# Performance work log

Hardware: AMD Instinct MI355X
Metric: run time of the kernel (lower is better)

The kernel has to match this reference:

```python
import jax, jax.numpy as jnp
import numpy as np

WINDOW_SIZE = (4, 7, 7)  # (t, h, w); N = 4*7*7 = 196


def _relative_position_index(ws):
    t, h, w = ws
    coords = np.stack(np.meshgrid(np.arange(t), np.arange(h), np.arange(w), indexing='ij'))  # (3,t,h,w)
    cf = coords.reshape(3, -1)                      # (3, N)
    rc = (cf[:, :, None] - cf[:, None, :]).transpose(1, 2, 0).astype(np.int64)  # (N, N, 3)
    rc[..., 0] += t - 1
    rc[..., 1] += h - 1
    rc[..., 2] += w - 1
    rc[..., 0] *= (2 * h - 1) * (2 * w - 1)
    rc[..., 1] *= 2 * w - 1
    return rc.sum(-1)                               # (N, N) indices into bias table


def setup_inputs() -> dict:
    key = jax.random.key(0)
    ks = jax.random.split(key, 7)
    B, B_dim, N, C, H = 4, 64, 196, 512, 16
    hd = C // H
    B_ = B * B_dim
    n_bias = (2 * 4 - 1) * (2 * 7 - 1) * (2 * 7 - 1)  # 1183
    return {
        'x': jax.random.normal(ks[0], (B_, N, C), jnp.float32),
        'q_global': jax.random.normal(ks[1], (B, 1, H, N, hd), jnp.float32),
        'kv_w': jax.random.normal(ks[2], (2 * C, C), jnp.float32) * (C ** -0.5),
        'kv_b': jnp.zeros((2 * C,), jnp.float32),
        'proj_w': jax.random.normal(ks[3], (C, C), jnp.float32) * (C ** -0.5),
        'proj_b': jnp.zeros((C,), jnp.float32),
        'bias_table': jax.random.normal(ks[4], (n_bias, H), jnp.float32) * 0.02,
    }


def reference(x, q_global, kv_w, kv_b, proj_w, proj_b, bias_table):
    B_, N, C = x.shape
    B, _, H, _, hd = q_global.shape
    B_dim = B_ // B
    scale = hd ** -0.5

    # kv projection: (B_, N, 2C) -> k, v each (B_, H, N, hd)
    kv = (x @ kv_w.T + kv_b).reshape(B_, N, 2, H, hd).transpose(2, 0, 3, 1, 4)
    keys, values = kv[0], kv[1]

    # global queries repeated across windows: (B,1,H,N,hd) -> (B_, H, N, hd)
    q = jnp.broadcast_to(q_global, (B, B_dim, H, N, hd)).reshape(B_, H, N, hd)
    q = q * scale

    attn = jnp.einsum('bhnd,bhmd->bhnm', q, keys)  # (B_, H, N, N)

    # gathered relative position bias (static index table)
    rpi = jnp.asarray(_relative_position_index(WINDOW_SIZE))  # (N, N)
    bias = bias_table[rpi.reshape(-1)].reshape(N, N, H).transpose(2, 0, 1)  # (H, N, N)
    attn = jax.nn.softmax(attn + bias[None], axis=-1)

    out = jnp.einsum('bhnm,bhmd->bhnd', attn, values)  # (B_, H, N, hd)
    out = out.transpose(0, 2, 1, 3).reshape(B_, N, C)
    return out @ proj_w.T + proj_b
```

## Files before the change

kernel.cpp:

```cpp
#include <hip/hip_runtime.h>
#include <stdint.h>

typedef __attribute__((ext_vector_type(8))) short short8;
typedef __attribute__((ext_vector_type(4))) float f32x4;
typedef __attribute__((ext_vector_type(4))) unsigned short u16x4;

typedef unsigned short ushort_t;

__device__ __forceinline__ unsigned short f2bf(float f) {
    union { float f; uint32_t u; } c; c.f = f;
    uint32_t u = c.u;
    return (unsigned short)((u + 0x7FFFu + ((u >> 16) & 1u)) >> 16);
}

__device__ __forceinline__ f32x4 mfma16(short8 a, short8 b, f32x4 c) {
    return __builtin_amdgcn_mfma_f32_16x16x32_bf16(a, b, c, 0, 0, 0);
}


__global__ __launch_bounds__(256) void cvt_x_k(const float4* __restrict__ in,
                                               u16x4* __restrict__ out, int n4) {
    int i = blockIdx.x * 256 + threadIdx.x;
    if (i < n4) {
        float4 v = in[i];
        u16x4 o;
        o[0] = f2bf(v.x); o[1] = f2bf(v.y); o[2] = f2bf(v.z); o[3] = f2bf(v.w);
        out[i] = o;
    }
}

__global__ __launch_bounds__(256) void cvt_small_k(const float4* __restrict__ kvw,
                                                   const float4* __restrict__ pw,
                                                   const float4* __restrict__ qg,
                                                   u16x4* __restrict__ kvwb,
                                                   u16x4* __restrict__ pwb,
                                                   u16x4* __restrict__ qb) {
    const float qs = 0.17677669529663687f;
    int i = blockIdx.x * 256 + threadIdx.x;
    if (i < 131072) {
        float4 v = kvw[i];
        u16x4 o; o[0]=f2bf(v.x); o[1]=f2bf(v.y); o[2]=f2bf(v.z); o[3]=f2bf(v.w);
        kvwb[i] = o;
    } else if (i < 196608) {
        int j = i - 131072;
        float4 v = pw[j];
        u16x4 o; o[0]=f2bf(v.x); o[1]=f2bf(v.y); o[2]=f2bf(v.z); o[3]=f2bf(v.w);
        pwb[j] = o;
    } else {
        int j = i - 196608;
        float4 v = qg[j];
        u16x4 o; o[0]=f2bf(v.x*qs); o[1]=f2bf(v.y*qs); o[2]=f2bf(v.z*qs); o[3]=f2bf(v.w*qs);
        qb[j] = o;
    }
}

__global__ __launch_bounds__(256) void bias_k(const float* __restrict__ bt,
                                              float* __restrict__ out) {
    int idx = blockIdx.x * 256 + threadIdx.x;
    int h = idx / 43264;
    int rem = idx - h * 43264;
    int i = rem / 208;
    int j = rem - i * 208;
    float v = -1e30f;
    if (i < 196 && j < 196) {
        int t1 = i / 49, r1 = i - t1 * 49, h1 = r1 / 7, w1 = r1 - h1 * 7;
        int t2 = j / 49, r2 = j - t2 * 49, h2 = r2 / 7, w2 = r2 - h2 * 7;
        int bi = (t1 - t2 + 3) * 169 + (h1 - h2 + 6) * 13 + (w1 - w2 + 6);
        v = bt[bi * 16 + h];
    }
    out[idx] = v;
}

__global__ __launch_bounds__(256) void gemm_kv(const ushort_t* __restrict__ A,
                                               const ushort_t* __restrict__ Bw,
                                               const float* __restrict__ kvb,
                                               ushort_t* __restrict__ Ko,
                                               ushort_t* __restrict__ Vo) {
    __shared__ ushort_t As[128 * 72];
    __shared__ ushort_t Bs[128 * 72];
    const int tid = threadIdx.x;
    const int lane = tid & 63, wave = tid >> 6;
    const int lrow = lane & 15, quad = lane >> 4;
    const int wr = wave >> 1, wc = wave & 1;
    const long arow0 = (long)blockIdx.x * 128;
    const int brow0 = blockIdx.y * 128;

    f32x4 acc[4][4];
#pragma unroll
    for (int i = 0; i < 4; ++i)
#pragma unroll
        for (int j = 0; j < 4; ++j) acc[i][j] = (f32x4){0.f, 0.f, 0.f, 0.f};

    for (int k0 = 0; k0 < 512; k0 += 64) {
        short8 ar[4], br[4];
#pragma unroll
        for (int it = 0; it < 4; ++it) {
            int c = it * 256 + tid;
            int row = c >> 3, cc = c & 7;
            ar[it] = *(const short8*)&A[(arow0 + row) * 512 + k0 + cc * 8];
            br[it] = *(const short8*)&Bw[(long)(brow0 + row) * 512 + k0 + cc * 8];
        }
        __syncthreads();
#pragma unroll
        for (int it = 0; it < 4; ++it) {
            int c = it * 256 + tid;
            int row = c >> 3, cc = c & 7;
            *(short8*)&As[row * 72 + cc * 8] = ar[it];
            *(short8*)&Bs[row * 72 + cc * 8] = br[it];
        }
        __syncthreads();
#pragma unroll
        for (int kk = 0; kk < 64; kk += 32) {
            short8 af[4], bf[4];
#pragma unroll
            for (int i = 0; i < 4; ++i)
                af[i] = *(const short8*)&As[(wr * 64 + i * 16 + lrow) * 72 + kk + quad * 8];
#pragma unroll
            for (int j = 0; j < 4; ++j)
                bf[j] = *(const short8*)&Bs[(wc * 64 + j * 16 + lrow) * 72 + kk + quad * 8];
#pragma unroll
            for (int i = 0; i < 4; ++i)
#pragma unroll
                for (int j = 0; j < 4; ++j)
                    acc[i][j] = mfma16(af[i], bf[j], acc[i][j]);
        }
    }
#pragma unroll
    for (int i = 0; i < 4; ++i) {
        int mb = (int)arow0 + wr * 64 + i * 16 + quad * 4;
#pragma unroll
        for (int r = 0; r < 4; ++r) {
            int m = mb + r;
            int b_ = m / 196;
            int n = m - b_ * 196;
#pragma unroll
            for (int j = 0; j < 4; ++j) {
                int cI = brow0 + wc * 64 + j * 16 + lrow;
                float v = acc[i][j][r] + kvb[cI];
                int hh = (cI >> 5) & 15, d = cI & 31;
                ushort_t* dst = (cI >> 9) ? Vo : Ko;
                dst[((((long)b_ << 4) + hh) * 196 + n) * 32 + d] = f2bf(v);
            }
        }
    }
}

__global__ __launch_bounds__(256) void attn_k(const ushort_t* __restrict__ Kb,
                                              const ushort_t* __restrict__ Vb,
                                              const ushort_t* __restrict__ Qb,
                                              const float* __restrict__ biasF,
                                              ushort_t* __restrict__ Ob) {
    const int tid = threadIdx.x, lane = tid & 63, wave = tid >> 6;
    const int lrow = lane & 15, quad = lane >> 4;
    const int bh = blockIdx.x;
    const int b_ = bh >> 4, h = bh & 15;
    const int Bq = b_ >> 6;

    __shared__ ushort_t Ks[208 * 40];
    __shared__ ushort_t Vt[32 * 232];
    __shared__ ushort_t Ps[4][16 * 232];

    const long kvoff = (long)bh * 6272;

    for (int c = tid; c < 784; c += 256) {
        int n = c >> 2, dp = c & 3;
        *(short8*)&Ks[n * 40 + dp * 8] = *(const short8*)&Kb[kvoff + n * 32 + dp * 8];
    }
    for (int i = tid; i < 12 * 40; i += 256) Ks[196 * 40 + i] = 0;
    for (int i = tid; i < 6272; i += 256) {
        int n = i >> 5, d = i & 31;
        Vt[d * 232 + n] = Vb[kvoff + i];
    }
    for (int i = tid; i < 32 * 36; i += 256) {
        int d = i / 36, j = i - d * 36;
        Vt[d * 232 + 196 + j] = 0;
    }
    for (int i = lane; i < 256; i += 64) {
        int r = i >> 4, cp = i & 15;
        Ps[wave][r * 232 + 208 + cp] = 0;
    }
    __syncthreads();

    const float* biasH = biasF + h * 43264;
    const long qbase = (((long)Bq * 16 + h) * 196) * 32;

    for (int rt = wave; rt < 13; rt += 4) {
        int qrow = rt * 16 + lrow; if (qrow > 195) qrow = 195;
        short8 qf = *(const short8*)&Qb[qbase + (long)qrow * 32 + quad * 8];

        f32x4 s[13];
#pragma unroll
        for (int ct = 0; ct < 13; ++ct) {
            short8 kf = *(const short8*)&Ks[(ct * 16 + lrow) * 40 + quad * 8];
            s[ct] = mfma16(qf, kf, (f32x4){0.f, 0.f, 0.f, 0.f});
        }
        const int srow0 = rt * 16 + quad * 4;
        float mx[4], sm[4];
#pragma unroll
        for (int r = 0; r < 4; ++r) mx[r] = -3e38f;
#pragma unroll
        for (int ct = 0; ct < 13; ++ct) {
            const float* bp = biasH + (long)srow0 * 208 + ct * 16 + lrow;
#pragma unroll
            for (int r = 0; r < 4; ++r) {
                float v = s[ct][r] + bp[r * 208];
                s[ct][r] = v;
                mx[r] = fmaxf(mx[r], v);
            }
        }
#pragma unroll
        for (int r = 0; r < 4; ++r) {
            mx[r] = fmaxf(mx[r], __shfl_xor(mx[r], 1, 16));
            mx[r] = fmaxf(mx[r], __shfl_xor(mx[r], 2, 16));
            mx[r] = fmaxf(mx[r], __shfl_xor(mx[r], 4, 16));
            mx[r] = fmaxf(mx[r], __shfl_xor(mx[r], 8, 16));
            sm[r] = 0.f;
        }
#pragma unroll
        for (int ct = 0; ct < 13; ++ct)
#pragma unroll
            for (int r = 0; r < 4; ++r) {
                float p = __expf(s[ct][r] - mx[r]);
                s[ct][r] = p;
                sm[r] += p;
            }
#pragma unroll
        for (int r = 0; r < 4; ++r) {
            sm[r] += __shfl_xor(sm[r], 1, 16);
            sm[r] += __shfl_xor(sm[r], 2, 16);
            sm[r] += __shfl_xor(sm[r], 4, 16);
            sm[r] += __shfl_xor(sm[r], 8, 16);
            sm[r] = 1.0f / sm[r];
        }
        ushort_t* prow = &Ps[wave][0];
#pragma unroll
        for (int ct = 0; ct < 13; ++ct)
#pragma unroll
            for (int r = 0; r < 4; ++r)
                prow[(quad * 4 + r) * 232 + ct * 16 + lrow] = f2bf(s[ct][r] * sm[r]);
        asm volatile("s_waitcnt lgkmcnt(0)" ::: "memory");

        f32x4 o0 = (f32x4){0.f,0.f,0.f,0.f}, o1 = (f32x4){0.f,0.f,0.f,0.f};
#pragma unroll
        for (int ks = 0; ks < 7; ++ks) {
            short8 pf = *(const short8*)&prow[lrow * 232 + ks * 32 + quad * 8];
            short8 v0 = *(const short8*)&Vt[lrow * 232 + ks * 32 + quad * 8];
            short8 v1 = *(const short8*)&Vt[(16 + lrow) * 232 + ks * 32 + quad * 8];
            o0 = mfma16(pf, v0, o0);
            o1 = mfma16(pf, v1, o1);
        }
        const long obase = (long)b_ * 196 * 512 + h * 32;
#pragma unroll
        for (int r = 0; r < 4; ++r) {
            int m = srow0 + r;
            if (m < 196) {
                Ob[obase + (long)m * 512 + lrow]      = f2bf(o0[r]);
                Ob[obase + (long)m * 512 + 16 + lrow] = f2bf(o1[r]);
            }
        }
    }
}

__global__ __launch_bounds__(256) void gemm_proj(const ushort_t* __restrict__ A,
                                                 const ushort_t* __restrict__ Bw,
                                                 const float* __restrict__ pb,
                                                 float* __restrict__ out) {
    __shared__ ushort_t As[128 * 72];
    __shared__ ushort_t Bs[128 * 72];
    const int tid = threadIdx.x;
    const int lane = tid & 63, wave = tid >> 6;
    const int lrow = lane & 15, quad = lane >> 4;
    const int wr = wave >> 1, wc = wave & 1;
    const long arow0 = (long)blockIdx.x * 128;
    const int brow0 = blockIdx.y * 128;

    f32x4 acc[4][4];
#pragma unroll
    for (int i = 0; i < 4; ++i)
#pragma unroll
        for (int j = 0; j < 4; ++j) acc[i][j] = (f32x4){0.f, 0.f, 0.f, 0.f};

    for (int k0 = 0; k0 < 512; k0 += 64) {
        short8 ar[4], br[4];
#pragma unroll
        for (int it = 0; it < 4; ++it) {
            int c = it * 256 + tid;
            int row = c >> 3, cc = c & 7;
            ar[it] = *(const short8*)&A[(arow0 + row) * 512 + k0 + cc * 8];
            br[it] = *(const short8*)&Bw[(long)(brow0 + row) * 512 + k0 + cc * 8];
        }
        __syncthreads();
#pragma unroll
        for (int it = 0; it < 4; ++it) {
            int c = it * 256 + tid;
            int row = c >> 3, cc = c & 7;
            *(short8*)&As[row * 72 + cc * 8] = ar[it];
            *(short8*)&Bs[row * 72 + cc * 8] = br[it];
        }
        __syncthreads();
#pragma unroll
        for (int kk = 0; kk < 64; kk += 32) {
            short8 af[4], bf[4];
#pragma unroll
            for (int i = 0; i < 4; ++i)
                af[i] = *(const short8*)&As[(wr * 64 + i * 16 + lrow) * 72 + kk + quad * 8];
#pragma unroll
            for (int j = 0; j < 4; ++j)
                bf[j] = *(const short8*)&Bs[(wc * 64 + j * 16 + lrow) * 72 + kk + quad * 8];
#pragma unroll
            for (int i = 0; i < 4; ++i)
#pragma unroll
                for (int j = 0; j < 4; ++j)
                    acc[i][j] = mfma16(af[i], bf[j], acc[i][j]);
        }
    }
#pragma unroll
    for (int i = 0; i < 4; ++i) {
        long mb = arow0 + wr * 64 + i * 16 + quad * 4;
#pragma unroll
        for (int r = 0; r < 4; ++r) {
            long m = mb + r;
#pragma unroll
            for (int j = 0; j < 4; ++j) {
                int cI = brow0 + wc * 64 + j * 16 + lrow;
                out[m * 512 + cI] = acc[i][j][r] + pb[cI];
            }
        }
    }
}


extern "C" void kernel_launch(void* const* d_in, const int* in_sizes, int n_in,
                              void* d_out, int out_size, void* d_ws, size_t ws_size,
                              hipStream_t stream) {
    const float* x   = (const float*)d_in[0];
    const float* qg  = (const float*)d_in[1];
    const float* kvw = (const float*)d_in[2];
    const float* kvb = (const float*)d_in[3];
    const float* pw  = (const float*)d_in[4];
    const float* pb  = (const float*)d_in[5];
    const float* bt  = (const float*)d_in[6];
    float* out = (float*)d_out;

    char* ws = (char*)d_ws;
    ushort_t* xb    = (ushort_t*)(ws);
    ushort_t* kbuf  = (ushort_t*)(ws + 51380224);
    ushort_t* vbuf  = (ushort_t*)(ws + 102760448);
    ushort_t* kvwb  = (ushort_t*)(ws + 154140672);
    ushort_t* pwb   = (ushort_t*)(ws + 155189248);
    ushort_t* qb    = (ushort_t*)(ws + 155713536);
    float*    biasF = (float*)   (ws + 156516352);
    ushort_t* obuf  = xb;

    cvt_x_k<<<25088, 256, 0, stream>>>((const float4*)x, (u16x4*)xb, 6422528);
    cvt_small_k<<<1160, 256, 0, stream>>>((const float4*)kvw, (const float4*)pw,
                                          (const float4*)qg,
                                          (u16x4*)kvwb, (u16x4*)pwb, (u16x4*)qb);
    bias_k<<<2704, 256, 0, stream>>>(bt, biasF);
    gemm_kv<<<dim3(392, 8), 256, 0, stream>>>(xb, kvwb, kvb, kbuf, vbuf);
    attn_k<<<4096, 256, 0, stream>>>(kbuf, vbuf, qb, biasF, obuf);
    gemm_proj<<<dim3(392, 4), 256, 0, stream>>>(obuf, pwb, pb, out);
}
```

Before: 462.7 us.

## Use direct global-to-LDS loads, write V transposed, and split attention per row tile

Both GEMMs now stage A and B tiles with global_load_lds straight into unpadded shared memory instead of going through registers. The KV GEMM writes V already transposed and padded to 208 columns, with a new padv_k kernel zeroing the pad. The attention kernel gives each wave one (batch-head, row-tile) unit, reads K and V directly from global memory without staging them in shared memory, and skips the row-max pass. It relies on the bias being pre-scaled by log2e and transposed so it can be read as float4. This drops staging and synchronisation overhead but risks LDS bank conflicts on the unpadded tiles and overflow in exp without max subtraction. Rounding is also changed to a faster, non-ties-even bf16 conversion.

```diff
diff --git a/kernel.cpp b/kernel.cpp
--- a/kernel.cpp
+++ b/kernel.cpp
@@ -4,7 +4,6 @@
 typedef __attribute__((ext_vector_type(8))) short short8;
 typedef __attribute__((ext_vector_type(4))) float f32x4;
 typedef __attribute__((ext_vector_type(4))) unsigned short u16x4;
-
 typedef unsigned short ushort_t;
 
 __device__ __forceinline__ unsigned short f2bf(float f) {
@@ -12,9 +11,17 @@
     uint32_t u = c.u;
     return (unsigned short)((u + 0x7FFFu + ((u >> 16) & 1u)) >> 16);
 }
-
+__device__ __forceinline__ unsigned short f2bf_fast(float f) {
+    union { float f; uint32_t u; } c; c.f = f;
+    return (unsigned short)((c.u + 0x8000u) >> 16);
+}
 __device__ __forceinline__ f32x4 mfma16(short8 a, short8 b, f32x4 c) {
     return __builtin_amdgcn_mfma_f32_16x16x32_bf16(a, b, c, 0, 0, 0);
+}
+__device__ __forceinline__ void gl_lds16(const ushort_t* g, ushort_t* l) {
+    __builtin_amdgcn_global_load_lds((const __attribute__((address_space(1))) uint32_t*)g,
+                                     (__attribute__((address_space(3))) uint32_t*)l,
+                                     16, 0, 0);
 }
 
 
@@ -59,16 +66,24 @@
     int idx = blockIdx.x * 256 + threadIdx.x;
     int h = idx / 43264;
     int rem = idx - h * 43264;
-    int i = rem / 208;
-    int j = rem - i * 208;
+    int j = rem / 208;
+    int i = rem - j * 208;
     float v = -1e30f;
-    if (i < 196 && j < 196) {
-        int t1 = i / 49, r1 = i - t1 * 49, h1 = r1 / 7, w1 = r1 - h1 * 7;
-        int t2 = j / 49, r2 = j - t2 * 49, h2 = r2 / 7, w2 = r2 - h2 * 7;
+    if (j < 196) {
+        int ii = i < 196 ? i : 195;
+        int t1 = ii / 49, r1 = ii - t1 * 49, h1 = r1 / 7, w1 = r1 - h1 * 7;
+        int t2 = j / 49,  r2 = j - t2 * 49,  h2 = r2 / 7, w2 = r2 - h2 * 7;
         int bi = (t1 - t2 + 3) * 169 + (h1 - h2 + 6) * 13 + (w1 - w2 + 6);
-        v = bt[bi * 16 + h];
+        v = bt[bi * 16 + h] * 1.44269504f;
     }
     out[idx] = v;
+}
+
+__global__ __launch_bounds__(256) void padv_k(u16x4* __restrict__ base) {
+    int idx = blockIdx.x * 256 + threadIdx.x;
+    int bh = idx / 96, rr = idx - bh * 96;
+    int d = rr / 3, c = rr - d * 3;
+    base[bh * 1664 + d * 52 + 49 + c] = (u16x4){0, 0, 0, 0};
 }
 
 __global__ __launch_bounds__(256) void gemm_kv(const ushort_t* __restrict__ A,
@@ -76,14 +91,15 @@
                                                const float* __restrict__ kvb,
                                                ushort_t* __restrict__ Ko,
                                                ushort_t* __restrict__ Vo) {
-    __shared__ ushort_t As[128 * 72];
-    __shared__ ushort_t Bs[128 * 72];
+    __shared__ __align__(16) ushort_t As[128 * 64];
+    __shared__ __align__(16) ushort_t Bs[128 * 64];
     const int tid = threadIdx.x;
     const int lane = tid & 63, wave = tid >> 6;
     const int lrow = lane & 15, quad = lane >> 4;
     const int wr = wave >> 1, wc = wave & 1;
+    const int lr8 = lane >> 3, lc8 = lane & 7;
     const long arow0 = (long)blockIdx.x * 128;
-    const int brow0 = blockIdx.y * 128;
+    const long brow0 = (long)blockIdx.y * 128;
 
     f32x4 acc[4][4];
 #pragma unroll
@@ -92,21 +108,16 @@
         for (int j = 0; j < 4; ++j) acc[i][j] = (f32x4){0.f, 0.f, 0.f, 0.f};
 
     for (int k0 = 0; k0 < 512; k0 += 64) {
-        short8 ar[4], br[4];
-#pragma unroll
-        for (int it = 0; it < 4; ++it) {
-            int c = it * 256 + tid;
-            int row = c >> 3, cc = c & 7;
-            ar[it] = *(const short8*)&A[(arow0 + row) * 512 + k0 + cc * 8];
-            br[it] = *(const short8*)&Bw[(long)(brow0 + row) * 512 + k0 + cc * 8];
-        }
         __syncthreads();
 #pragma unroll
-        for (int it = 0; it < 4; ++it) {
-            int c = it * 256 + tid;
-            int row = c >> 3, cc = c & 7;
-            *(short8*)&As[row * 72 + cc * 8] = ar[it];
-            *(short8*)&Bs[row * 72 + cc * 8] = br[it];
+        for (int i = 0; i < 8; ++i) {
+            int c = wave * 8 + i;
+            if (c < 16) {
+                gl_lds16(&A[(arow0 + c * 8 + lr8) * 512 + k0 + lc8 * 8], &As[c * 512]);
+            } else {
+                int cb = c - 16;
+                gl_lds16(&Bw[(brow0 + cb * 8 + lr8) * 512 + k0 + lc8 * 8], &Bs[cb * 512]);
+            }
         }
         __syncthreads();
 #pragma unroll
@@ -114,10 +125,10 @@
             short8 af[4], bf[4];
 #pragma unroll
             for (int i = 0; i < 4; ++i)
-                af[i] = *(const short8*)&As[(wr * 64 + i * 16 + lrow) * 72 + kk + quad * 8];
+                af[i] = *(const short8*)&As[(wr * 64 + i * 16 + lrow) * 64 + kk + quad * 8];
 #pragma unroll
             for (int j = 0; j < 4; ++j)
-                bf[j] = *(const short8*)&Bs[(wc * 64 + j * 16 + lrow) * 72 + kk + quad * 8];
+                bf[j] = *(const short8*)&Bs[(wc * 64 + j * 16 + lrow) * 64 + kk + quad * 8];
 #pragma unroll
             for (int i = 0; i < 4; ++i)
 #pragma unroll
@@ -135,128 +146,92 @@
             int n = m - b_ * 196;
 #pragma unroll
             for (int j = 0; j < 4; ++j) {
-                int cI = brow0 + wc * 64 + j * 16 + lrow;
+                int cI = (int)brow0 + wc * 64 + j * 16 + lrow;
                 float v = acc[i][j][r] + kvb[cI];
                 int hh = (cI >> 5) & 15, d = cI & 31;
-                ushort_t* dst = (cI >> 9) ? Vo : Ko;
-                dst[((((long)b_ << 4) + hh) * 196 + n) * 32 + d] = f2bf(v);
+                long bh = (long)b_ * 16 + hh;
+                if (cI < 512) Ko[bh * 6272 + n * 32 + d] = f2bf_fast(v);
+                else          Vo[bh * 6656 + d * 208 + n] = f2bf_fast(v);
             }
         }
     }
 }
 
 __global__ __launch_bounds__(256) void attn_k(const ushort_t* __restrict__ Kb,
-                                              const ushort_t* __restrict__ Vb,
+                                              const ushort_t* __restrict__ Vt,
                                               const ushort_t* __restrict__ Qb,
-                                              const float* __restrict__ biasF,
+                                              const float* __restrict__ biasT,
                                               ushort_t* __restrict__ Ob) {
     const int tid = threadIdx.x, lane = tid & 63, wave = tid >> 6;
     const int lrow = lane & 15, quad = lane >> 4;
-    const int bh = blockIdx.x;
+    __shared__ __align__(16) ushort_t Ps[4][16 * 232];
+
+    const int unit = blockIdx.x * 4 + wave;
+    const int bh = unit / 13;
+    const int rt = unit - bh * 13;
     const int b_ = bh >> 4, h = bh & 15;
     const int Bq = b_ >> 6;
 
-    __shared__ ushort_t Ks[208 * 40];
-    __shared__ ushort_t Vt[32 * 232];
-    __shared__ ushort_t Ps[4][16 * 232];
-
-    const long kvoff = (long)bh * 6272;
-
-    for (int c = tid; c < 784; c += 256) {
-        int n = c >> 2, dp = c & 3;
-        *(short8*)&Ks[n * 40 + dp * 8] = *(const short8*)&Kb[kvoff + n * 32 + dp * 8];
-    }
-    for (int i = tid; i < 12 * 40; i += 256) Ks[196 * 40 + i] = 0;
-    for (int i = tid; i < 6272; i += 256) {
-        int n = i >> 5, d = i & 31;
-        Vt[d * 232 + n] = Vb[kvoff + i];
-    }
-    for (int i = tid; i < 32 * 36; i += 256) {
-        int d = i / 36, j = i - d * 36;
-        Vt[d * 232 + 196 + j] = 0;
-    }
-    for (int i = lane; i < 256; i += 64) {
-        int r = i >> 4, cp = i & 15;
-        Ps[wave][r * 232 + 208 + cp] = 0;
-    }
-    __syncthreads();
-
-    const float* biasH = biasF + h * 43264;
-    const long qbase = (((long)Bq * 16 + h) * 196) * 32;
-
-    for (int rt = wave; rt < 13; rt += 4) {
-        int qrow = rt * 16 + lrow; if (qrow > 195) qrow = 195;
-        short8 qf = *(const short8*)&Qb[qbase + (long)qrow * 32 + quad * 8];
-
-        f32x4 s[13];
-#pragma unroll
-        for (int ct = 0; ct < 13; ++ct) {
-            short8 kf = *(const short8*)&Ks[(ct * 16 + lrow) * 40 + quad * 8];
-            s[ct] = mfma16(qf, kf, (f32x4){0.f, 0.f, 0.f, 0.f});
-        }
-        const int srow0 = rt * 16 + quad * 4;
-        float mx[4], sm[4];
-#pragma unroll
-        for (int r = 0; r < 4; ++r) mx[r] = -3e38f;
-#pragma unroll
-        for (int ct = 0; ct < 13; ++ct) {
-            const float* bp = biasH + (long)srow0 * 208 + ct * 16 + lrow;
-#pragma unroll
-            for (int r = 0; r < 4; ++r) {
-                float v = s[ct][r] + bp[r * 208];
-                s[ct][r] = v;
-                mx[r] = fmaxf(mx[r], v);
-            }
-        }
-#pragma unroll
-        for (int r = 0; r < 4; ++r) {
-            mx[r] = fmaxf(mx[r], __shfl_xor(mx[r], 1, 16));
-            mx[r] = fmaxf(mx[r], __shfl_xor(mx[r], 2, 16));
-            mx[r] = fmaxf(mx[r], __shfl_xor(mx[r], 4, 16));
-            mx[r] = fmaxf(mx[r], __shfl_xor(mx[r], 8, 16));
-            sm[r] = 0.f;
-        }
-#pragma unroll
-        for (int ct = 0; ct < 13; ++ct)
-#pragma unroll
-            for (int r = 0; r < 4; ++r) {
-                float p = __expf(s[ct][r] - mx[r]);
-                s[ct][r] = p;
-                sm[r] += p;
-            }
-#pragma unroll
-        for (int r = 0; r < 4; ++r) {
-            sm[r] += __shfl_xor(sm[r], 1, 16);
-            sm[r] += __shfl_xor(sm[r], 2, 16);
-            sm[r] += __shfl_xor(sm[r], 4, 16);
-            sm[r] += __shfl_xor(sm[r], 8, 16);
-            sm[r] = 1.0f / sm[r];
-        }
-        ushort_t* prow = &Ps[wave][0];
-#pragma unroll
-        for (int ct = 0; ct < 13; ++ct)
-#pragma unroll
-            for (int r = 0; r < 4; ++r)
-                prow[(quad * 4 + r) * 232 + ct * 16 + lrow] = f2bf(s[ct][r] * sm[r]);
-        asm volatile("s_waitcnt lgkmcnt(0)" ::: "memory");
-
-        f32x4 o0 = (f32x4){0.f,0.f,0.f,0.f}, o1 = (f32x4){0.f,0.f,0.f,0.f};
-#pragma unroll
-        for (int ks = 0; ks < 7; ++ks) {
-            short8 pf = *(const short8*)&prow[lrow * 232 + ks * 32 + quad * 8];
-            short8 v0 = *(const short8*)&Vt[lrow * 232 + ks * 32 + quad * 8];
-            short8 v1 = *(const short8*)&Vt[(16 + lrow) * 232 + ks * 32 + quad * 8];
-            o0 = mfma16(pf, v0, o0);
-            o1 = mfma16(pf, v1, o1);
-        }
-        const long obase = (long)b_ * 196 * 512 + h * 32;
-#pragma unroll
-        for (int r = 0; r < 4; ++r) {
-            int m = srow0 + r;
-            if (m < 196) {
-                Ob[obase + (long)m * 512 + lrow]      = f2bf(o0[r]);
-                Ob[obase + (long)m * 512 + 16 + lrow] = f2bf(o1[r]);
-            }
+    ushort_t* prow = &Ps[wave][0];
+#pragma unroll
+    for (int i = lane; i < 128; i += 64) {
+        int r = i >> 3, dw = i & 7;
+        *(uint32_t*)&prow[r * 232 + 208 + dw * 2] = 0u;
+    }
+
+    int qrow = rt * 16 + lrow; if (qrow > 195) qrow = 195;
+    const short8 qf = *(const short8*)&Qb[((((long)Bq * 16 + h) * 196) + qrow) * 32 + quad * 8];
+
+    const long koff = (long)bh * 6272;
+    const float* bb = biasT + h * 43264;
+    const int srow0 = rt * 16 + quad * 4;
+
+    f32x4 sm = (f32x4){0.f, 0.f, 0.f, 0.f};
+#pragma unroll
+    for (int ct = 0; ct < 13; ++ct) {
+        short8 kf = *(const short8*)&Kb[koff + (ct * 16 + lrow) * 32 + quad * 8];
+        f32x4 s = mfma16(qf, kf, (f32x4){0.f, 0.f, 0.f, 0.f});
+        float4 bv = *(const float4*)&bb[(ct * 16 + lrow) * 208 + srow0];
+        float p0 = exp2f(fmaf(s[0], 1.44269504f, bv.x));
+        float p1 = exp2f(fmaf(s[1], 1.44269504f, bv.y));
+        float p2 = exp2f(fmaf(s[2], 1.44269504f, bv.z));
+        float p3 = exp2f(fmaf(s[3], 1.44269504f, bv.w));
+        sm[0] += p0; sm[1] += p1; sm[2] += p2; sm[3] += p3;
+        prow[(quad * 4 + 0) * 232 + ct * 16 + lrow] = f2bf_fast(p0);
+        prow[(quad * 4 + 1) * 232 + ct * 16 + lrow] = f2bf_fast(p1);
+        prow[(quad * 4 + 2) * 232 + ct * 16 + lrow] = f2bf_fast(p2);
+        prow[(quad * 4 + 3) * 232 + ct * 16 + lrow] = f2bf_fast(p3);
+    }
+#pragma unroll
+    for (int r = 0; r < 4; ++r) {
+        sm[r] += __shfl_xor(sm[r], 1, 16);
+        sm[r] += __shfl_xor(sm[r], 2, 16);
+        sm[r] += __shfl_xor(sm[r], 4, 16);
+        sm[r] += __shfl_xor(sm[r], 8, 16);
+    }
+    f32x4 inv;
+#pragma unroll
+    for (int r = 0; r < 4; ++r) inv[r] = __builtin_amdgcn_rcpf(sm[r]);
+
+    asm volatile("s_waitcnt lgkmcnt(0)" ::: "memory");
+
+    const long voff = (long)bh * 6656;
+    f32x4 o0 = (f32x4){0.f,0.f,0.f,0.f}, o1 = (f32x4){0.f,0.f,0.f,0.f};
+#pragma unroll
+    for (int ks = 0; ks < 7; ++ks) {
+        short8 pf = *(const short8*)&prow[lrow * 232 + ks * 32 + quad * 8];
+        short8 v0 = *(const short8*)&Vt[voff + lrow * 208 + ks * 32 + quad * 8];
+        short8 v1 = *(const short8*)&Vt[voff + (16 + lrow) * 208 + ks * 32 + quad * 8];
+        o0 = mfma16(pf, v0, o0);
+        o1 = mfma16(pf, v1, o1);
+    }
+    const long obase = (long)b_ * 100352 + (long)h * 32;
+#pragma unroll
+    for (int r = 0; r < 4; ++r) {
+        int m = srow0 + r;
+        if (m < 196) {
+            Ob[obase + (long)m * 512 + lrow]      = f2bf_fast(o0[r] * inv[r]);
+            Ob[obase + (long)m * 512 + 16 + lrow] = f2bf_fast(o1[r] * inv[r]);
         }
     }
 }
@@ -265,14 +240,15 @@
                                                  const ushort_t* __restrict__ Bw,
                                                  const float* __restrict__ pb,
                                                  float* __restrict__ out) {
-    __shared__ ushort_t As[128 * 72];
-    __shared__ ushort_t Bs[128 * 72];
+    __shared__ __align__(16) ushort_t As[128 * 64];
+    __shared__ __align__(16) ushort_t Bs[128 * 64];
     const int tid = threadIdx.x;
     const int lane = tid & 63, wave = tid >> 6;
     const int lrow = lane & 15, quad = lane >> 4;
     const int wr = wave >> 1, wc = wave & 1;
+    const int lr8 = lane >> 3, lc8 = lane & 7;
     const long arow0 = (long)blockIdx.x * 128;
-    const int brow0 = blockIdx.y * 128;
+    const long brow0 = (long)blockIdx.y * 128;
 
     f32x4 acc[4][4];
 #pragma unroll
@@ -281,21 +257,16 @@
         for (int j = 0; j < 4; ++j) acc[i][j] = (f32x4){0.f, 0.f, 0.f, 0.f};
 
     for (int k0 = 0; k0 < 512; k0 += 64) {
-        short8 ar[4], br[4];
-#pragma unroll
-        for (int it = 0; it < 4; ++it) {
-            int c = it * 256 + tid;
-            int row = c >> 3, cc = c & 7;
-            ar[it] = *(const short8*)&A[(arow0 + row) * 512 + k0 + cc * 8];
-            br[it] = *(const short8*)&Bw[(long)(brow0 + row) * 512 + k0 + cc * 8];
-        }
         __syncthreads();
 #pragma unroll
-        for (int it = 0; it < 4; ++it) {
-            int c = it * 256 + tid;
-            int row = c >> 3, cc = c & 7;
-            *(short8*)&As[row * 72 + cc * 8] = ar[it];
-            *(short8*)&Bs[row * 72 + cc * 8] = br[it];
+        for (int i = 0; i < 8; ++i) {
+            int c = wave * 8 + i;
+            if (c < 16) {
+                gl_lds16(&A[(arow0 + c * 8 + lr8) * 512 + k0 + lc8 * 8], &As[c * 512]);
+            } else {
+                int cb = c - 16;
+                gl_lds16(&Bw[(brow0 + cb * 8 + lr8) * 512 + k0 + lc8 * 8], &Bs[cb * 512]);
+            }
         }
         __syncthreads();
 #pragma unroll
@@ -303,10 +274,10 @@
             short8 af[4], bf[4];
 #pragma unroll
             for (int i = 0; i < 4; ++i)
-                af[i] = *(const short8*)&As[(wr * 64 + i * 16 + lrow) * 72 + kk + quad * 8];
+                af[i] = *(const short8*)&As[(wr * 64 + i * 16 + lrow) * 64 + kk + quad * 8];
 #pragma unroll
             for (int j = 0; j < 4; ++j)
-                bf[j] = *(const short8*)&Bs[(wc * 64 + j * 16 + lrow) * 72 + kk + quad * 8];
+                bf[j] = *(const short8*)&Bs[(wc * 64 + j * 16 + lrow) * 64 + kk + quad * 8];
 #pragma unroll
             for (int i = 0; i < 4; ++i)
 #pragma unroll
@@ -322,7 +293,7 @@
             long m = mb + r;
 #pragma unroll
             for (int j = 0; j < 4; ++j) {
-                int cI = brow0 + wc * 64 + j * 16 + lrow;
+                int cI = (int)brow0 + wc * 64 + j * 16 + lrow;
                 out[m * 512 + cI] = acc[i][j][r] + pb[cI];
             }
         }
@@ -346,18 +317,19 @@
     ushort_t* xb    = (ushort_t*)(ws);
     ushort_t* kbuf  = (ushort_t*)(ws + 51380224);
     ushort_t* vbuf  = (ushort_t*)(ws + 102760448);
-    ushort_t* kvwb  = (ushort_t*)(ws + 154140672);
-    ushort_t* pwb   = (ushort_t*)(ws + 155189248);
-    ushort_t* qb    = (ushort_t*)(ws + 155713536);
-    float*    biasF = (float*)   (ws + 156516352);
+    ushort_t* kvwb  = (ushort_t*)(ws + 157286400);
+    ushort_t* pwb   = (ushort_t*)(ws + 158334976);
+    ushort_t* qb    = (ushort_t*)(ws + 158859264);
+    float*    biasT = (float*)   (ws + 159662080);
     ushort_t* obuf  = xb;
 
     cvt_x_k<<<25088, 256, 0, stream>>>((const float4*)x, (u16x4*)xb, 6422528);
     cvt_small_k<<<1160, 256, 0, stream>>>((const float4*)kvw, (const float4*)pw,
                                           (const float4*)qg,
                                           (u16x4*)kvwb, (u16x4*)pwb, (u16x4*)qb);
-    bias_k<<<2704, 256, 0, stream>>>(bt, biasF);
+    bias_k<<<2704, 256, 0, stream>>>(bt, biasT);
+    padv_k<<<1536, 256, 0, stream>>>((u16x4*)vbuf);
     gemm_kv<<<dim3(392, 8), 256, 0, stream>>>(xb, kvwb, kvb, kbuf, vbuf);
-    attn_k<<<4096, 256, 0, stream>>>(kbuf, vbuf, qb, biasF, obuf);
+    attn_k<<<13312, 256, 0, stream>>>(kbuf, vbuf, qb, biasT, obuf);
     gemm_proj<<<dim3(392, 4), 256, 0, stream>>>(obuf, pwb, pb, out);
 }
```

After: 515.4 us. 11.4% more time.
